# Optimization experiments

Hardware: AMD Instinct MI355X
Metric: run time of the kernel (lower is better)

Reference implementation:

```python
import jax, jax.numpy as jnp
import numpy as np

B, T, N, D = 8, 24, 96, 32   # batch, timesteps, objects, per-object feature dim
H = 512                       # hidden_dim = cfg.MODEL.HIDDEN_SIZE * 2

def _linear_init(key, fan_in, fan_out):
    kw, kb = jax.random.split(key)
    s = 1.0 / np.sqrt(fan_in)
    W = jax.random.uniform(kw, (fan_in, fan_out), jnp.float32, -s, s)
    b = jax.random.uniform(kb, (fan_out,), jnp.float32, -s, s)
    return W, b

def setup_inputs() -> dict:
    key = jax.random.key(0)
    ks = jax.random.split(key, 8)
    x = jax.random.normal(ks[0], (B, T, N, D), jnp.float32)
    W_enc, b_enc = _linear_init(ks[1], 6 * D, H)
    W1, b1 = _linear_init(ks[2], H, H)
    W2, b2 = _linear_init(ks[3], H, H)
    W3, b3 = _linear_init(ks[4], H, H)
    Wd1, bd1 = _linear_init(ks[5], H, H)
    Wd2, bd2 = _linear_init(ks[6], H, D)
    return {"x": x, "W_enc": W_enc, "b_enc": b_enc, "W1": W1, "b1": b1,
            "W2": W2, "b2": b2, "W3": W3, "b3": b3,
            "Wd1": Wd1, "bd1": bd1, "Wd2": Wd2, "bd2": bd2}

def reference(x, W_enc, b_enc, W1, b1, W2, b2, W3, b3, Wd1, bd1, Wd2, bd2):
    relu = jax.nn.relu

    def int_net(s):  # s: [B, N, 3D] (concat of 3 past states)
        n = s.shape[1]
        e1 = jnp.broadcast_to(s[:, :, None, :], (s.shape[0], n, n, s.shape[-1]))
        e2 = jnp.broadcast_to(s[:, None, :, :], (s.shape[0], n, n, s.shape[-1]))
        pc = jnp.concatenate([e1, e2], axis=-1)          # [B, N, N, 6D]
        h = relu(pc @ W_enc + b_enc)
        h = relu(h @ W1 + b1)
        h = relu(h @ W2 + b2)
        emb = (h @ W3 + b3).mean(axis=2)                  # [B, N, H]
        return relu(emb @ Wd1 + bd1) @ Wd2 + bd2          # [B, N, D]

    z = jnp.zeros((B, N, D), jnp.float32)

    def step(carry, xt):  # xt: [B, N, D]
        p1, p2, p3 = carry
        exist = xt[:, :, 1:2]
        s = exist * xt + (1.0 - exist) * p3
        past = (p2, p3, s)
        out = int_net(jnp.concatenate(past, axis=-1))
        return past, out

    _, outs = jax.lax.scan(step, (z, z, z), jnp.swapaxes(x, 0, 1))  # outs: [T, B, N, D]
    return jnp.swapaxes(outs[:-1], 0, 1)  # [B, T-1, N, D]
```

## Files before the change

kernel.cpp:

```cpp
#include <hip/hip_runtime.h>

#define DEVI __device__ __forceinline__

typedef __bf16 bf16x8 __attribute__((ext_vector_type(8)));
typedef float  f32x4  __attribute__((ext_vector_type(4)));

static constexpr int Bb = 8, Tt = 24, Nn = 96, Dd = 32;
static constexpr int TO = 23;
static constexpr int TB = TO * Bb;
static constexpr int ROWS = TB * Nn;

DEVI unsigned short f2bf(float f) {
  union { float f; unsigned u; } v; v.f = f;
  unsigned r = v.u + 0x7FFFu + ((v.u >> 16) & 1u);
  return (unsigned short)(r >> 16);
}
DEVI float bf2f(unsigned short u) {
  union { unsigned u; float f; } v; v.u = (unsigned)u << 16; return v.f;
}

__global__ void pack_kernel(const float* __restrict__ W, unsigned short* __restrict__ dst,
                            int K, int N) {
  int p = blockIdx.x * 256 + threadIdx.x;
  if (p >= K * N) return;
  int j = p & 7, lane = (p >> 3) & 63, pb = p >> 9;
  int NB = N >> 4;
  int nb = pb % NB, kb = pb / NB;
  int k = kb * 32 + ((lane >> 4) << 3) + j;
  int n = nb * 16 + (lane & 15);
  dst[p] = f2bf(W[(size_t)k * N + n]);
}

__global__ void s3_kernel(const float* __restrict__ x, unsigned short* __restrict__ S3) {
  int tid = blockIdx.x * 256 + threadIdx.x;
  int b = tid / (Nn * Dd), n = (tid / Dd) % Nn, d = tid % Dd;
  auto idx = [&](int t, int k) { return ((size_t)((t * Bb + b) * Nn + n)) * 96 + k; };
  S3[idx(0, d)] = 0; S3[idx(0, 32 + d)] = 0; S3[idx(1, d)] = 0;
  float s = 0.f;
  for (int t = 0; t < TO; ++t) {
    const float* xr = x + ((size_t)(b * Tt + t) * Nn + n) * Dd;
    float e = xr[1];
    s = e * xr[d] + (1.f - e) * s;
    unsigned short sb = f2bf(s);
    S3[idx(t, 64 + d)] = sb;
    if (t + 1 < TO) S3[idx(t + 1, 32 + d)] = sb;
    if (t + 2 < TO) S3[idx(t + 2, d)] = sb;
  }
}

__global__ __launch_bounds__(512, 2) void uv_kernel(
    const unsigned short* __restrict__ S3, const unsigned short* __restrict__ WpE,
    const float* __restrict__ bE,
    unsigned short* __restrict__ U, unsigned short* __restrict__ V) {
  __shared__ unsigned short sS[96 * 104];
  int tid = threadIdx.x, lane = tid & 63, w = tid >> 6;
  int tb = blockIdx.x;
  const unsigned short* s3t = S3 + (size_t)tb * (96 * 96);
  for (int c = tid; c < 96 * 12; c += 512) {
    int j = c / 12, kc = (c % 12) * 8;
    *(bf16x8*)(sS + j * 104 + kc) = *(const bf16x8*)(s3t + j * 96 + kc);
  }
  __syncthreads();
#pragma unroll
  for (int half = 0; half < 2; ++half) {
    f32x4 acc[6][4];
#pragma unroll
    for (int m = 0; m < 6; ++m)
#pragma unroll
      for (int n = 0; n < 4; ++n) acc[m][n] = f32x4{0.f, 0.f, 0.f, 0.f};
#pragma unroll
    for (int kb = 0; kb < 3; ++kb) {
      bf16x8 a[6], b[4];
#pragma unroll
      for (int m = 0; m < 6; ++m) {
        int row = 16 * m + (lane & 15);
        a[m] = *(const bf16x8*)(sS + row * 104 + kb * 32 + ((lane >> 4) << 3));
      }
#pragma unroll
      for (int n = 0; n < 4; ++n)
        b[n] = *(const bf16x8*)(WpE + ((size_t)(((half * 3 + kb) * 32 + w * 4 + n) * 64 + lane) << 3));
#pragma unroll
      for (int n = 0; n < 4; ++n)
#pragma unroll
        for (int m = 0; m < 6; ++m)
          acc[m][n] = __builtin_amdgcn_mfma_f32_16x16x32_bf16(a[m], b[n], acc[m][n], 0, 0, 0);
    }
    unsigned short* dst = half ? V : U;
#pragma unroll
    for (int n = 0; n < 4; ++n) {
      int col = 64 * w + 16 * n + (lane & 15);
      float bias = half ? 0.f : bE[col];
#pragma unroll
      for (int m = 0; m < 6; ++m)
#pragma unroll
        for (int r = 0; r < 4; ++r) {
          int row = 16 * m + ((lane >> 4) << 2) + r;
          dst[((size_t)tb * 96 + row) * 512 + col] = f2bf(acc[m][n][r] + bias);
        }
    }
  }
}

template <int KB, int NFR>
DEVI void run_layer(const unsigned short* sA, const unsigned short* wp,
                    int NB, int nb0, int lane, int phase, f32x4 acc[6][NFR]) {
  const char* sab = (const char*)sA;
  const char* bb  = (const char*)wp + ((size_t)(nb0 * 64 + lane) << 4);
  const int kstride = NB << 10;
  bf16x8 bq[3][NFR];
#pragma unroll
  for (int d = 0; d < 3; ++d)
#pragma unroll
    for (int n = 0; n < NFR; ++n)
      bq[d][n] = *(const bf16x8*)(bb + ((phase + d) & (KB - 1)) * kstride + (n << 10));
#pragma unroll
  for (int kb = 0; kb < KB; ++kb) {
    const int slot = kb % 3;
    int kbp = (kb + phase) & (KB - 1);
    bf16x8 a[6];
#pragma unroll
    for (int m = 0; m < 6; ++m) {
      int row = 16 * m + (lane & 15);
      int boff = (row * 1024 + kbp * 64 + ((lane >> 4) << 4)) ^ ((row & 7) << 4);
      a[m] = *(const bf16x8*)(sab + boff);
    }
#pragma unroll
    for (int n = 0; n < NFR; ++n)
#pragma unroll
      for (int m = 0; m < 6; ++m)
        acc[m][n] = __builtin_amdgcn_mfma_f32_16x16x32_bf16(a[m], bq[slot][n], acc[m][n], 0, 0, 0);
    if (kb + 3 < KB) {
      int kbn = (kb + 3 + phase) & (KB - 1);
      const char* b2 = bb + kbn * kstride;
#pragma unroll
      for (int n = 0; n < NFR; ++n)
        bq[slot][n] = *(const bf16x8*)(b2 + (n << 10));
    }
  }
}

template <int NFR>
DEVI void zacc(f32x4 (&acc)[6][NFR]) {
#pragma unroll
  for (int m = 0; m < 6; ++m)
#pragma unroll
    for (int n = 0; n < NFR; ++n) acc[m][n] = f32x4{0.f, 0.f, 0.f, 0.f};
}

template <bool RELU>
DEVI void epilogue_to_lds(unsigned short* sA, const float* __restrict__ bias,
                          int w, int lane, f32x4 acc[6][4]) {
  float bn[4];
#pragma unroll
  for (int n = 0; n < 4; ++n) bn[n] = bias[64 * w + 16 * n + (lane & 15)];
  __syncthreads();
  char* sab = (char*)sA;
#pragma unroll
  for (int m = 0; m < 6; ++m)
#pragma unroll
    for (int n = 0; n < 4; ++n)
#pragma unroll
      for (int r = 0; r < 4; ++r) {
        float v = acc[m][n][r] + bn[n];
        if (RELU) v = fmaxf(v, 0.f);
        int row = 16 * m + ((lane >> 4) << 2) + r;
        int boff = (row * 1024 + (64 * w + 16 * n + (lane & 15)) * 2) ^ ((row & 7) << 4);
        *(unsigned short*)(sab + boff) = f2bf(v);
      }
  __syncthreads();
}

__global__ __launch_bounds__(512)
__attribute__((amdgpu_waves_per_eu(2, 2))) void pair_kernel(
    const unsigned short* __restrict__ U, const unsigned short* __restrict__ V,
    const unsigned short* __restrict__ Wp1, const float* __restrict__ b1,
    const unsigned short* __restrict__ Wp2, const float* __restrict__ b2,
    unsigned short* __restrict__ hbar) {
  __shared__ unsigned short sA[96 * 512];
  int tid = threadIdx.x, lane = tid & 63, w = tid >> 6;
  int gid = blockIdx.x;
  int tb = gid / 96;
  int phase = gid & 15;
  const unsigned short* Up = U + (size_t)gid * 512;
  const unsigned short* Vp = V + (size_t)tb * (96 * 512);
  int kc = tid & 63;
  int j0 = tid >> 6;
  float u[8];
  {
    bf16x8 u8 = *(const bf16x8*)(Up + kc * 8);
#pragma unroll
    for (int l = 0; l < 8; ++l) u[l] = bf2f(((const unsigned short*)&u8)[l]);
  }
#pragma unroll
  for (int half = 0; half < 2; ++half) {
    bf16x8 vv[6];
#pragma unroll
    for (int it = 0; it < 6; ++it)
      vv[it] = *(const bf16x8*)(Vp + (size_t)(j0 + (half * 6 + it) * 8) * 512 + kc * 8);
#pragma unroll
    for (int it = 0; it < 6; ++it) {
      int j = j0 + (half * 6 + it) * 8;
      unsigned short h[8];
#pragma unroll
      for (int l = 0; l < 8; ++l)
        h[l] = f2bf(fmaxf(u[l] + bf2f(((const unsigned short*)&vv[it])[l]), 0.f));
      int boff = (j * 1024 + kc * 16) ^ ((j & 7) << 4);
      *(bf16x8*)((char*)sA + boff) = *(bf16x8*)h;
    }
  }
  __syncthreads();
  f32x4 acc[6][4];
  zacc(acc); run_layer<16, 4>(sA, Wp1, 32, w * 4, lane, phase, acc);
  epilogue_to_lds<true>(sA, b1, w, lane, acc);
  zacc(acc); run_layer<16, 4>(sA, Wp2, 32, w * 4, lane, phase, acc);
  float p[4];
#pragma unroll
  for (int n = 0; n < 4; ++n) {
    float bn = b2[64 * w + 16 * n + (lane & 15)];
    float s = 0.f;
#pragma unroll
    for (int m = 0; m < 6; ++m)
#pragma unroll
      for (int r = 0; r < 4; ++r) s += fmaxf(acc[m][n][r] + bn, 0.f);
    p[n] = s;
  }
#pragma unroll
  for (int n = 0; n < 4; ++n) {
    p[n] += __shfl_xor(p[n], 16);
    p[n] += __shfl_xor(p[n], 32);
  }
  int g = lane >> 4;
  float sel = g == 0 ? p[0] : g == 1 ? p[1] : g == 2 ? p[2] : p[3];
  hbar[(size_t)gid * 512 + 64 * w + lane] = f2bf(sel * (1.f / 96.f));
}

__global__ __launch_bounds__(512)
__attribute__((amdgpu_waves_per_eu(2, 2))) void decode_kernel(
    const unsigned short* __restrict__ hbar,
    const unsigned short* __restrict__ Wp3, const float* __restrict__ b3,
    const unsigned short* __restrict__ WpD1, const float* __restrict__ bd1,
    const unsigned short* __restrict__ WpD2, const float* __restrict__ bd2,
    float* __restrict__ out) {
  __shared__ unsigned short sA[96 * 512];
  int tid = threadIdx.x, lane = tid & 63, w = tid >> 6;
  int r0 = blockIdx.x * 96;
  int phase = blockIdx.x & 15;
  for (int c = tid; c < 96 * 64; c += 512) {
    int j = c / 64, kc = (c % 64) * 8;
    bf16x8 v = *(const bf16x8*)(hbar + (size_t)(r0 + j) * 512 + kc);
    int boff = (j * 1024 + kc * 2) ^ ((j & 7) << 4);
    *(bf16x8*)((char*)sA + boff) = v;
  }
  __syncthreads();
  f32x4 acc[6][4];
  zacc(acc); run_layer<16, 4>(sA, Wp3, 32, w * 4, lane, phase, acc);
  epilogue_to_lds<false>(sA, b3, w, lane, acc);
  zacc(acc); run_layer<16, 4>(sA, WpD1, 32, w * 4, lane, phase, acc);
  epilogue_to_lds<true>(sA, bd1, w, lane, acc);
  if (w == 0) {
    f32x4 acc2[6][2];
    zacc(acc2); run_layer<16, 2>(sA, WpD2, 2, 0, lane, phase, acc2);
#pragma unroll
    for (int n = 0; n < 2; ++n) {
      float bn = bd2[16 * n + (lane & 15)];
#pragma unroll
      for (int m = 0; m < 6; ++m)
#pragma unroll
        for (int r = 0; r < 4; ++r) {
          int row = 16 * m + ((lane >> 4) << 2) + r;
          int R = r0 + row;
          int t = R / 768, b = (R / 96) & 7, i = R % 96;
          out[(((size_t)b * TO + t) * 96 + i) * 32 + 16 * n + (lane & 15)] =
              acc2[m][n][r] + bn;
        }
    }
  }
}

extern "C" void kernel_launch(void* const* d_in, const int* in_sizes, int n_in,
                              void* d_out, int out_size, void* d_ws, size_t ws_size,
                              hipStream_t stream) {
  const float* x     = (const float*)d_in[0];
  const float* W_enc = (const float*)d_in[1];
  const float* b_enc = (const float*)d_in[2];
  const float* W1    = (const float*)d_in[3];
  const float* b1    = (const float*)d_in[4];
  const float* W2    = (const float*)d_in[5];
  const float* b2    = (const float*)d_in[6];
  const float* W3    = (const float*)d_in[7];
  const float* b3    = (const float*)d_in[8];
  const float* Wd1   = (const float*)d_in[9];
  const float* bd1   = (const float*)d_in[10];
  const float* Wd2   = (const float*)d_in[11];
  const float* bd2   = (const float*)d_in[12];
  float* out = (float*)d_out;

  char* ws = (char*)d_ws;
  size_t off = 0;
  auto alloc = [&](size_t bytes) {
    char* p = ws + off;
    off += (bytes + 255) & ~(size_t)255;
    return p;
  };
  unsigned short* S3    = (unsigned short*)alloc((size_t)TB * 96 * 96 * 2);
  unsigned short* Ub    = (unsigned short*)alloc((size_t)ROWS * 512 * 2);
  unsigned short* Vb    = (unsigned short*)alloc((size_t)ROWS * 512 * 2);
  unsigned short* hbar  = (unsigned short*)alloc((size_t)ROWS * 512 * 2);
  unsigned short* WpE   = (unsigned short*)alloc((size_t)192 * 512 * 2);
  unsigned short* Wp1p  = (unsigned short*)alloc((size_t)512 * 512 * 2);
  unsigned short* Wp2p  = (unsigned short*)alloc((size_t)512 * 512 * 2);
  unsigned short* Wp3p  = (unsigned short*)alloc((size_t)512 * 512 * 2);
  unsigned short* WpD1p = (unsigned short*)alloc((size_t)512 * 512 * 2);
  unsigned short* WpD2p = (unsigned short*)alloc((size_t)512 * 32 * 2);

  pack_kernel<<<(192 * 512) / 256, 256, 0, stream>>>(W_enc, WpE, 192, 512);
  pack_kernel<<<(512 * 512) / 256, 256, 0, stream>>>(W1, Wp1p, 512, 512);
  pack_kernel<<<(512 * 512) / 256, 256, 0, stream>>>(W2, Wp2p, 512, 512);
  pack_kernel<<<(512 * 512) / 256, 256, 0, stream>>>(W3, Wp3p, 512, 512);
  pack_kernel<<<(512 * 512) / 256, 256, 0, stream>>>(Wd1, WpD1p, 512, 512);
  pack_kernel<<<(512 * 32) / 256, 256, 0, stream>>>(Wd2, WpD2p, 512, 32);
  s3_kernel<<<96, 256, 0, stream>>>(x, S3);
  uv_kernel<<<TB, 512, 0, stream>>>(S3, WpE, b_enc, Ub, Vb);
  pair_kernel<<<ROWS, 512, 0, stream>>>(Ub, Vb, Wp1p, b1, Wp2p, b2, hbar);
  decode_kernel<<<TB, 512, 0, stream>>>(hbar, Wp3p, b3, WpD1p, bd1, WpD2p, bd2, out);
  (void)in_sizes; (void)n_in; (void)out_size; (void)ws_size;
}
```

Before: 1.545 ms.

## Use 1024-thread blocks with half-width warp tiles in pair and decode kernels

Doubles the block size of the pair and decode kernels to 16 waves, so each wave computes two 16-column fragments instead of four, which halves accumulator registers. The weight prefetch depth drops from three stages to two, and the LDS XOR swizzle widens from 8 to 16 rows. The aim is more resident waves to hide latency on the MFMA-bound layers. In exchange, each A-fragment load from LDS is reused across fewer MFMAs, so LDS read traffic per block doubles, and the shallower prefetch leaves less time to hide weight-load latency.

```diff
diff --git a/kernel.cpp b/kernel.cpp
--- a/kernel.cpp
+++ b/kernel.cpp
@@ -107,21 +107,21 @@
   const char* sab = (const char*)sA;
   const char* bb  = (const char*)wp + ((size_t)(nb0 * 64 + lane) << 4);
   const int kstride = NB << 10;
-  bf16x8 bq[3][NFR];
-#pragma unroll
-  for (int d = 0; d < 3; ++d)
+  bf16x8 bq[2][NFR];
+#pragma unroll
+  for (int d = 0; d < 2; ++d)
 #pragma unroll
     for (int n = 0; n < NFR; ++n)
       bq[d][n] = *(const bf16x8*)(bb + ((phase + d) & (KB - 1)) * kstride + (n << 10));
 #pragma unroll
   for (int kb = 0; kb < KB; ++kb) {
-    const int slot = kb % 3;
+    const int slot = kb & 1;
     int kbp = (kb + phase) & (KB - 1);
     bf16x8 a[6];
 #pragma unroll
     for (int m = 0; m < 6; ++m) {
       int row = 16 * m + (lane & 15);
-      int boff = (row * 1024 + kbp * 64 + ((lane >> 4) << 4)) ^ ((row & 7) << 4);
+      int boff = (row * 1024 + kbp * 64 + ((lane >> 4) << 4)) ^ ((row & 15) << 4);
       a[m] = *(const bf16x8*)(sab + boff);
     }
 #pragma unroll
@@ -129,8 +129,8 @@
 #pragma unroll
       for (int m = 0; m < 6; ++m)
         acc[m][n] = __builtin_amdgcn_mfma_f32_16x16x32_bf16(a[m], bq[slot][n], acc[m][n], 0, 0, 0);
-    if (kb + 3 < KB) {
-      int kbn = (kb + 3 + phase) & (KB - 1);
+    if (kb + 2 < KB) {
+      int kbn = (kb + 2 + phase) & (KB - 1);
       const char* b2 = bb + kbn * kstride;
 #pragma unroll
       for (int n = 0; n < NFR; ++n)
@@ -147,31 +147,30 @@
     for (int n = 0; n < NFR; ++n) acc[m][n] = f32x4{0.f, 0.f, 0.f, 0.f};
 }
 
-template <bool RELU>
+template <bool RELU, int NFR>
 DEVI void epilogue_to_lds(unsigned short* sA, const float* __restrict__ bias,
-                          int w, int lane, f32x4 acc[6][4]) {
-  float bn[4];
-#pragma unroll
-  for (int n = 0; n < 4; ++n) bn[n] = bias[64 * w + 16 * n + (lane & 15)];
+                          int w, int lane, f32x4 acc[6][NFR]) {
+  float bn[NFR];
+#pragma unroll
+  for (int n = 0; n < NFR; ++n) bn[n] = bias[16 * NFR * w + 16 * n + (lane & 15)];
   __syncthreads();
   char* sab = (char*)sA;
 #pragma unroll
   for (int m = 0; m < 6; ++m)
 #pragma unroll
-    for (int n = 0; n < 4; ++n)
+    for (int n = 0; n < NFR; ++n)
 #pragma unroll
       for (int r = 0; r < 4; ++r) {
         float v = acc[m][n][r] + bn[n];
         if (RELU) v = fmaxf(v, 0.f);
         int row = 16 * m + ((lane >> 4) << 2) + r;
-        int boff = (row * 1024 + (64 * w + 16 * n + (lane & 15)) * 2) ^ ((row & 7) << 4);
+        int boff = (row * 1024 + (16 * NFR * w + 16 * n + (lane & 15)) * 2) ^ ((row & 15) << 4);
         *(unsigned short*)(sab + boff) = f2bf(v);
       }
   __syncthreads();
 }
 
-__global__ __launch_bounds__(512)
-__attribute__((amdgpu_waves_per_eu(2, 2))) void pair_kernel(
+__global__ __launch_bounds__(1024, 4) void pair_kernel(
     const unsigned short* __restrict__ U, const unsigned short* __restrict__ V,
     const unsigned short* __restrict__ Wp1, const float* __restrict__ b1,
     const unsigned short* __restrict__ Wp2, const float* __restrict__ b2,
@@ -191,32 +190,29 @@
 #pragma unroll
     for (int l = 0; l < 8; ++l) u[l] = bf2f(((const unsigned short*)&u8)[l]);
   }
-#pragma unroll
-  for (int half = 0; half < 2; ++half) {
-    bf16x8 vv[6];
-#pragma unroll
-    for (int it = 0; it < 6; ++it)
-      vv[it] = *(const bf16x8*)(Vp + (size_t)(j0 + (half * 6 + it) * 8) * 512 + kc * 8);
-#pragma unroll
-    for (int it = 0; it < 6; ++it) {
-      int j = j0 + (half * 6 + it) * 8;
-      unsigned short h[8];
-#pragma unroll
-      for (int l = 0; l < 8; ++l)
-        h[l] = f2bf(fmaxf(u[l] + bf2f(((const unsigned short*)&vv[it])[l]), 0.f));
-      int boff = (j * 1024 + kc * 16) ^ ((j & 7) << 4);
-      *(bf16x8*)((char*)sA + boff) = *(bf16x8*)h;
-    }
-  }
-  __syncthreads();
-  f32x4 acc[6][4];
-  zacc(acc); run_layer<16, 4>(sA, Wp1, 32, w * 4, lane, phase, acc);
-  epilogue_to_lds<true>(sA, b1, w, lane, acc);
-  zacc(acc); run_layer<16, 4>(sA, Wp2, 32, w * 4, lane, phase, acc);
-  float p[4];
-#pragma unroll
-  for (int n = 0; n < 4; ++n) {
-    float bn = b2[64 * w + 16 * n + (lane & 15)];
+  bf16x8 vv[6];
+#pragma unroll
+  for (int it = 0; it < 6; ++it)
+    vv[it] = *(const bf16x8*)(Vp + (size_t)(j0 + it * 16) * 512 + kc * 8);
+#pragma unroll
+  for (int it = 0; it < 6; ++it) {
+    int j = j0 + it * 16;
+    unsigned short h[8];
+#pragma unroll
+    for (int l = 0; l < 8; ++l)
+      h[l] = f2bf(fmaxf(u[l] + bf2f(((const unsigned short*)&vv[it])[l]), 0.f));
+    int boff = (j * 1024 + kc * 16) ^ ((j & 15) << 4);
+    *(bf16x8*)((char*)sA + boff) = *(bf16x8*)h;
+  }
+  __syncthreads();
+  f32x4 acc[6][2];
+  zacc(acc); run_layer<16, 2>(sA, Wp1, 32, w * 2, lane, phase, acc);
+  epilogue_to_lds<true, 2>(sA, b1, w, lane, acc);
+  zacc(acc); run_layer<16, 2>(sA, Wp2, 32, w * 2, lane, phase, acc);
+  float p[2];
+#pragma unroll
+  for (int n = 0; n < 2; ++n) {
+    float bn = b2[32 * w + 16 * n + (lane & 15)];
     float s = 0.f;
 #pragma unroll
     for (int m = 0; m < 6; ++m)
@@ -225,17 +221,18 @@
     p[n] = s;
   }
 #pragma unroll
-  for (int n = 0; n < 4; ++n) {
+  for (int n = 0; n < 2; ++n) {
     p[n] += __shfl_xor(p[n], 16);
     p[n] += __shfl_xor(p[n], 32);
   }
   int g = lane >> 4;
-  float sel = g == 0 ? p[0] : g == 1 ? p[1] : g == 2 ? p[2] : p[3];
-  hbar[(size_t)gid * 512 + 64 * w + lane] = f2bf(sel * (1.f / 96.f));
-}
-
-__global__ __launch_bounds__(512)
-__attribute__((amdgpu_waves_per_eu(2, 2))) void decode_kernel(
+  if (g < 2) {
+    float sel = (g & 1) ? p[1] : p[0];
+    hbar[(size_t)gid * 512 + 32 * w + (g & 1) * 16 + (lane & 15)] = f2bf(sel * (1.f / 96.f));
+  }
+}
+
+__global__ __launch_bounds__(1024, 4) void decode_kernel(
     const unsigned short* __restrict__ hbar,
     const unsigned short* __restrict__ Wp3, const float* __restrict__ b3,
     const unsigned short* __restrict__ WpD1, const float* __restrict__ bd1,
@@ -245,18 +242,18 @@
   int tid = threadIdx.x, lane = tid & 63, w = tid >> 6;
   int r0 = blockIdx.x * 96;
   int phase = blockIdx.x & 15;
-  for (int c = tid; c < 96 * 64; c += 512) {
-    int j = c / 64, kc = (c % 64) * 8;
-    bf16x8 v = *(const bf16x8*)(hbar + (size_t)(r0 + j) * 512 + kc);
-    int boff = (j * 1024 + kc * 2) ^ ((j & 7) << 4);
+  for (int c = tid; c < 96 * 64; c += 1024) {
+    int j = c >> 6, kc = c & 63;
+    bf16x8 v = *(const bf16x8*)(hbar + (size_t)(r0 + j) * 512 + kc * 8);
+    int boff = (j * 1024 + kc * 16) ^ ((j & 15) << 4);
     *(bf16x8*)((char*)sA + boff) = v;
   }
   __syncthreads();
-  f32x4 acc[6][4];
-  zacc(acc); run_layer<16, 4>(sA, Wp3, 32, w * 4, lane, phase, acc);
-  epilogue_to_lds<false>(sA, b3, w, lane, acc);
-  zacc(acc); run_layer<16, 4>(sA, WpD1, 32, w * 4, lane, phase, acc);
-  epilogue_to_lds<true>(sA, bd1, w, lane, acc);
+  f32x4 acc[6][2];
+  zacc(acc); run_layer<16, 2>(sA, Wp3, 32, w * 2, lane, phase, acc);
+  epilogue_to_lds<false, 2>(sA, b3, w, lane, acc);
+  zacc(acc); run_layer<16, 2>(sA, WpD1, 32, w * 2, lane, phase, acc);
+  epilogue_to_lds<true, 2>(sA, bd1, w, lane, acc);
   if (w == 0) {
     f32x4 acc2[6][2];
     zacc(acc2); run_layer<16, 2>(sA, WpD2, 2, 0, lane, phase, acc2);
@@ -321,7 +318,7 @@
   pack_kernel<<<(512 * 32) / 256, 256, 0, stream>>>(Wd2, WpD2p, 512, 32);
   s3_kernel<<<96, 256, 0, stream>>>(x, S3);
   uv_kernel<<<TB, 512, 0, stream>>>(S3, WpE, b_enc, Ub, Vb);
-  pair_kernel<<<ROWS, 512, 0, stream>>>(Ub, Vb, Wp1p, b1, Wp2p, b2, hbar);
-  decode_kernel<<<TB, 512, 0, stream>>>(hbar, Wp3p, b3, WpD1p, bd1, WpD2p, bd2, out);
+  pair_kernel<<<ROWS, 1024, 0, stream>>>(Ub, Vb, Wp1p, b1, Wp2p, b2, hbar);
+  decode_kernel<<<TB, 1024, 0, stream>>>(hbar, Wp3p, b3, WpD1p, bd1, WpD2p, bd2, out);
   (void)in_sizes; (void)n_in; (void)out_size; (void)ws_size;
 }
```

Result: slower. 2.739 ms (+77.3%).
